# Kernel optimization log

Hardware: AMD Instinct MI355X
Metric: run time of the kernel (lower is better)

Reference implementation:

```python
import jax, jax.numpy as jnp
import numpy as np

T = 400      # timestamps (window length chosen == timestamps -> no padding branch)
D = 10000    # out_dimension (HDC hypervector dim)
TWO_PI = 2.0 * np.pi


def setup_inputs() -> dict:
    key = jax.random.key(0)
    ks = jax.random.split(key, 10)
    # monotonically increasing timestamps so jerk dt > 0
    t = jnp.cumsum(jax.random.uniform(ks[0], (T,), jnp.float32) + 0.5)
    xyz = jax.random.normal(ks[1], (T, 3), jnp.float32)
    inp = jnp.concatenate([t[:, None], xyz], axis=1)  # [T,4] = (t, x, y, z)
    W1 = jax.random.normal(ks[2], (D, T * 3), jnp.float32)
    b1 = jax.random.uniform(ks[3], (D,), jnp.float32, 0.0, TWO_PI)
    W2 = jax.random.normal(ks[4], (D, T * 3), jnp.float32)
    b2 = jax.random.uniform(ks[5], (D,), jnp.float32, 0.0, TWO_PI)
    W3 = jax.random.normal(ks[6], (D, T * 2), jnp.float32)
    b3 = jax.random.uniform(ks[7], (D,), jnp.float32, 0.0, TWO_PI)
    W4 = jax.random.normal(ks[8], (D, 3), jnp.float32)
    b4 = jax.random.uniform(ks[9], (D,), jnp.float32, 0.0, TWO_PI)
    return {"input": inp, "W1": W1, "b1": b1, "W2": W2, "b2": b2,
            "W3": W3, "b3": b3, "W4": W4, "b4": b4}


def _hypertangent(x, W, b):
    # HyperTangent random-feature embedding: tanh(W @ x + b)
    return jnp.tanh(W @ x + b)


def reference(input, W1, b1, W2, b2, W3, b3, W4, b4):
    t = input[:, 0] - input[0, 0]           # zero-base the time column
    xyz = input[:, 1:]                      # [T,3]
    sq = xyz * xyz
    mags = jnp.sqrt(jnp.sum(sq, axis=1))    # [T]
    energy = jnp.sum(sq, axis=0) / xyz.shape[0]  # [3]
    # vectorized jerk: (x_{i+1}-x_i)/(t_{i+1}-t_i), with a leading zeros row
    dt = (t[1:] - t[:-1])[:, None]          # [T-1,1]
    jerks = jnp.concatenate(
        [jnp.zeros((1, 3), input.dtype), (xyz[1:] - xyz[:-1]) / dt], axis=0)  # [T,3]
    jerk_mags = jnp.sqrt(jnp.sum(jerks * jerks, axis=1))  # [T]
    # window == timestamps -> no padding path
    features1 = jnp.concatenate([xyz[:, 0], xyz[:, 1], xyz[:, 2]])      # [3T]
    features2 = jnp.concatenate([jerks[:, 0], jerks[:, 1], jerks[:, 2]])  # [3T]
    features3 = jnp.concatenate([mags, jerk_mags])                       # [2T]
    hv1 = _hypertangent(features1, W1, b1)
    hv2 = _hypertangent(features2, W2, b2)
    hv3 = _hypertangent(features3, W3, b3)
    hv4 = _hypertangent(energy, W4, b4)
    return jnp.tanh(hv1 * hv4 + hv2 + hv3)  # [D]
```

## Files before the change

### kernel.cpp

```cpp
#include <hip/hip_runtime.h>
#include <hip/hip_bf16.h>
#include <math.h>

#define T_PTS 400
#define D_OUT 10000
#define L12   1200
#define L3    800
#define FEAT_TOTAL (L12 + L12 + L3 + 3)

__global__ __launch_bounds__(512)
void hdc_features_kernel(const float* __restrict__ in, float* __restrict__ feat) {
    __shared__ float red[3][8];
    const int tid = threadIdx.x;
    float ex = 0.f, ey = 0.f, ez = 0.f;

    if (tid < T_PTS) {
        const float4 cur = reinterpret_cast<const float4*>(in)[tid];
        const float x = cur.y, y = cur.z, z = cur.w;
        feat[tid]        = x;
        feat[400 + tid]  = y;
        feat[800 + tid]  = z;
        feat[2400 + tid] = sqrtf(x * x + y * y + z * z);
        ex = x * x; ey = y * y; ez = z * z;

        float jx = 0.f, jy = 0.f, jz = 0.f;
        if (tid > 0) {
            const float4 prev = reinterpret_cast<const float4*>(in)[tid - 1];
            const float dt = cur.x - prev.x;
            const float inv = 1.0f / dt;
            jx = (x - prev.y) * inv;
            jy = (y - prev.z) * inv;
            jz = (z - prev.w) * inv;
        }
        feat[1200 + tid] = jx;
        feat[1600 + tid] = jy;
        feat[2000 + tid] = jz;
        feat[2800 + tid] = sqrtf(jx * jx + jy * jy + jz * jz);
    }

    #pragma unroll
    for (int off = 32; off; off >>= 1) {
        ex += __shfl_down(ex, off, 64);
        ey += __shfl_down(ey, off, 64);
        ez += __shfl_down(ez, off, 64);
    }
    const int wave = tid >> 6, lane = tid & 63;
    if (lane == 0) { red[0][wave] = ex; red[1][wave] = ey; red[2][wave] = ez; }
    __syncthreads();
    if (tid == 0) {
        float sx = 0.f, sy = 0.f, sz = 0.f;
        #pragma unroll
        for (int w = 0; w < 8; ++w) { sx += red[0][w]; sy += red[1][w]; sz += red[2][w]; }
        const float invT = 1.0f / (float)T_PTS;
        feat[3200] = sx * invT;
        feat[3201] = sy * invT;
        feat[3202] = sz * invT;
    }
}

__global__ __launch_bounds__(256)
void hdc_gemv_kernel(const float* __restrict__ W1, const float* __restrict__ b1,
                     const float* __restrict__ W2, const float* __restrict__ b2,
                     const float* __restrict__ W3, const float* __restrict__ b3,
                     const float* __restrict__ W4, const float* __restrict__ b4,
                     const float* __restrict__ feat, float* __restrict__ out) {
    __shared__ float f[FEAT_TOTAL];
    const int tid = threadIdx.x;
    for (int k = tid; k < FEAT_TOTAL; k += 256) f[k] = feat[k];
    __syncthreads();

    const float e0 = f[3200], e1 = f[3201], e2 = f[3202];
    const int wave = tid >> 6, lane = tid & 63;
    const int d0 = blockIdx.x * 8 + wave * 2;
    const int d1 = d0 + 1;

    const float* __restrict__ f1 = f;
    const float* __restrict__ f2 = f + 1200;
    const float* __restrict__ f3 = f + 2400;

    const float* __restrict__ w1a = W1 + (size_t)d0 * L12;
    const float* __restrict__ w1b = W1 + (size_t)d1 * L12;
    const float* __restrict__ w2a = W2 + (size_t)d0 * L12;
    const float* __restrict__ w2b = W2 + (size_t)d1 * L12;
    const float* __restrict__ w3a = W3 + (size_t)d0 * L3;
    const float* __restrict__ w3b = W3 + (size_t)d1 * L3;

    float a1a = 0.f, a1b = 0.f, a2a = 0.f, a2b = 0.f, a3a = 0.f, a3b = 0.f;

    for (int k = lane * 4; k < L3; k += 256) {
        const float s1x = f1[k], s1y = f1[k + 1], s1z = f1[k + 2], s1w = f1[k + 3];
        const float s2x = f2[k], s2y = f2[k + 1], s2z = f2[k + 2], s2w = f2[k + 3];
        const float s3x = f3[k], s3y = f3[k + 1], s3z = f3[k + 2], s3w = f3[k + 3];
        const float4 va = *reinterpret_cast<const float4*>(w1a + k);
        const float4 vb = *reinterpret_cast<const float4*>(w1b + k);
        const float4 vc = *reinterpret_cast<const float4*>(w2a + k);
        const float4 vd = *reinterpret_cast<const float4*>(w2b + k);
        const float4 ve = *reinterpret_cast<const float4*>(w3a + k);
        const float4 vf = *reinterpret_cast<const float4*>(w3b + k);
        a1a += va.x * s1x + va.y * s1y + va.z * s1z + va.w * s1w;
        a1b += vb.x * s1x + vb.y * s1y + vb.z * s1z + vb.w * s1w;
        a2a += vc.x * s2x + vc.y * s2y + vc.z * s2z + vc.w * s2w;
        a2b += vd.x * s2x + vd.y * s2y + vd.z * s2z + vd.w * s2w;
        a3a += ve.x * s3x + ve.y * s3y + ve.z * s3z + ve.w * s3w;
        a3b += vf.x * s3x + vf.y * s3y + vf.z * s3z + vf.w * s3w;
    }
    for (int k = L3 + lane * 4; k < L12; k += 256) {
        const float s1x = f1[k], s1y = f1[k + 1], s1z = f1[k + 2], s1w = f1[k + 3];
        const float s2x = f2[k], s2y = f2[k + 1], s2z = f2[k + 2], s2w = f2[k + 3];
        const float4 va = *reinterpret_cast<const float4*>(w1a + k);
        const float4 vb = *reinterpret_cast<const float4*>(w1b + k);
        const float4 vc = *reinterpret_cast<const float4*>(w2a + k);
        const float4 vd = *reinterpret_cast<const float4*>(w2b + k);
        a1a += va.x * s1x + va.y * s1y + va.z * s1z + va.w * s1w;
        a1b += vb.x * s1x + vb.y * s1y + vb.z * s1z + vb.w * s1w;
        a2a += vc.x * s2x + vc.y * s2y + vc.z * s2z + vc.w * s2w;
        a2b += vd.x * s2x + vd.y * s2y + vd.z * s2z + vd.w * s2w;
    }

    #pragma unroll
    for (int off = 32; off; off >>= 1) {
        a1a += __shfl_down(a1a, off, 64);
        a1b += __shfl_down(a1b, off, 64);
        a2a += __shfl_down(a2a, off, 64);
        a2b += __shfl_down(a2b, off, 64);
        a3a += __shfl_down(a3a, off, 64);
        a3b += __shfl_down(a3b, off, 64);
    }

    if (lane == 0) {
        const float hv1a = tanhf(a1a + b1[d0]);
        const float hv2a = tanhf(a2a + b2[d0]);
        const float hv3a = tanhf(a3a + b3[d0]);
        const float hv4a = tanhf(W4[(size_t)d0 * 3 + 0] * e0 +
                                 W4[(size_t)d0 * 3 + 1] * e1 +
                                 W4[(size_t)d0 * 3 + 2] * e2 + b4[d0]);
        out[d0] = tanhf(hv1a * hv4a + hv2a + hv3a);

        const float hv1b = tanhf(a1b + b1[d1]);
        const float hv2b = tanhf(a2b + b2[d1]);
        const float hv3b = tanhf(a3b + b3[d1]);
        const float hv4b = tanhf(W4[(size_t)d1 * 3 + 0] * e0 +
                                 W4[(size_t)d1 * 3 + 1] * e1 +
                                 W4[(size_t)d1 * 3 + 2] * e2 + b4[d1]);
        out[d1] = tanhf(hv1b * hv4b + hv2b + hv3b);
    }
}

extern "C" void kernel_launch(void* const* d_in, const int* in_sizes, int n_in,
                              void* d_out, int out_size, void* d_ws, size_t ws_size,
                              hipStream_t stream) {
    const float* input = (const float*)d_in[0];
    const float* W1 = (const float*)d_in[1];
    const float* b1 = (const float*)d_in[2];
    const float* W2 = (const float*)d_in[3];
    const float* b2 = (const float*)d_in[4];
    const float* W3 = (const float*)d_in[5];
    const float* b3 = (const float*)d_in[6];
    const float* W4 = (const float*)d_in[7];
    const float* b4 = (const float*)d_in[8];
    float* out = (float*)d_out;
    float* feat = (float*)d_ws;

    hdc_features_kernel<<<1, 512, 0, stream>>>(input, feat);
    hdc_gemv_kernel<<<D_OUT / 8, 256, 0, stream>>>(W1, b1, W2, b2, W3, b3,
                                                   W4, b4, feat, out);
}
```

Before: 167.2 us.

## Issue all weight loads upfront into registers and pad shared features for float4 reads

The GEMV kernel now issues every row's float4 weight loads into register arrays before any arithmetic, putting all loads for a lane in flight at once instead of a loop-carried load/compute sequence. The shared feature vectors are copied into zero-padded, aligned segments so they can be read as float4 with no bounds checks. Launch bounds are raised to request four blocks per CU. The cost is much higher register pressure, which could cause spills or lower occupancy.

```diff
diff --git a/kernel.cpp b/kernel.cpp
--- a/kernel.cpp
+++ b/kernel.cpp
@@ -7,6 +7,12 @@
 #define L12   1200
 #define L3    800
 #define FEAT_TOTAL (L12 + L12 + L3 + 3)
+
+#define F1_OFF 0
+#define F2_OFF 1280
+#define F3_OFF 2560
+#define E_OFF  3584
+#define FS_TOTAL 3587
 
 __global__ __launch_bounds__(512)
 void hdc_features_kernel(const float* __restrict__ in, float* __restrict__ feat) {
@@ -58,25 +64,28 @@
     }
 }
 
-__global__ __launch_bounds__(256)
+__global__ __launch_bounds__(256, 4)
 void hdc_gemv_kernel(const float* __restrict__ W1, const float* __restrict__ b1,
                      const float* __restrict__ W2, const float* __restrict__ b2,
                      const float* __restrict__ W3, const float* __restrict__ b3,
                      const float* __restrict__ W4, const float* __restrict__ b4,
                      const float* __restrict__ feat, float* __restrict__ out) {
-    __shared__ float f[FEAT_TOTAL];
+    __shared__ float fs[FS_TOTAL];
     const int tid = threadIdx.x;
-    for (int k = tid; k < FEAT_TOTAL; k += 256) f[k] = feat[k];
+
+    for (int k = tid; k < 1280; k += 256) {
+        fs[F1_OFF + k] = (k < L12) ? feat[k] : 0.f;
+        fs[F2_OFF + k] = (k < L12) ? feat[L12 + k] : 0.f;
+    }
+    for (int k = tid; k < 1024; k += 256)
+        fs[F3_OFF + k] = (k < L3) ? feat[2400 + k] : 0.f;
+    if (tid < 3) fs[E_OFF + tid] = feat[3200 + tid];
     __syncthreads();
 
-    const float e0 = f[3200], e1 = f[3201], e2 = f[3202];
     const int wave = tid >> 6, lane = tid & 63;
     const int d0 = blockIdx.x * 8 + wave * 2;
     const int d1 = d0 + 1;
-
-    const float* __restrict__ f1 = f;
-    const float* __restrict__ f2 = f + 1200;
-    const float* __restrict__ f3 = f + 2400;
+    const int k0 = lane * 4;
 
     const float* __restrict__ w1a = W1 + (size_t)d0 * L12;
     const float* __restrict__ w1b = W1 + (size_t)d1 * L12;
@@ -85,36 +94,55 @@
     const float* __restrict__ w3a = W3 + (size_t)d0 * L3;
     const float* __restrict__ w3b = W3 + (size_t)d1 * L3;
 
+    const bool v12 = (lane < 44);
+    const bool v3  = (lane < 8);
+    const float4 z4 = make_float4(0.f, 0.f, 0.f, 0.f);
+
+    float4 r1a[5], r1b[5], r2a[5], r2b[5], r3a[4], r3b[4];
+    #pragma unroll
+    for (int i = 0; i < 4; ++i) {
+        const int k = k0 + 256 * i;
+        r1a[i] = *reinterpret_cast<const float4*>(w1a + k);
+        r1b[i] = *reinterpret_cast<const float4*>(w1b + k);
+        r2a[i] = *reinterpret_cast<const float4*>(w2a + k);
+        r2b[i] = *reinterpret_cast<const float4*>(w2b + k);
+    }
+    {
+        const int k = k0 + 1024;
+        r1a[4] = v12 ? *reinterpret_cast<const float4*>(w1a + k) : z4;
+        r1b[4] = v12 ? *reinterpret_cast<const float4*>(w1b + k) : z4;
+        r2a[4] = v12 ? *reinterpret_cast<const float4*>(w2a + k) : z4;
+        r2b[4] = v12 ? *reinterpret_cast<const float4*>(w2b + k) : z4;
+    }
+    #pragma unroll
+    for (int i = 0; i < 3; ++i) {
+        const int k = k0 + 256 * i;
+        r3a[i] = *reinterpret_cast<const float4*>(w3a + k);
+        r3b[i] = *reinterpret_cast<const float4*>(w3b + k);
+    }
+    {
+        const int k = k0 + 768;
+        r3a[3] = v3 ? *reinterpret_cast<const float4*>(w3a + k) : z4;
+        r3b[3] = v3 ? *reinterpret_cast<const float4*>(w3b + k) : z4;
+    }
+
     float a1a = 0.f, a1b = 0.f, a2a = 0.f, a2b = 0.f, a3a = 0.f, a3b = 0.f;
-
-    for (int k = lane * 4; k < L3; k += 256) {
-        const float s1x = f1[k], s1y = f1[k + 1], s1z = f1[k + 2], s1w = f1[k + 3];
-        const float s2x = f2[k], s2y = f2[k + 1], s2z = f2[k + 2], s2w = f2[k + 3];
-        const float s3x = f3[k], s3y = f3[k + 1], s3z = f3[k + 2], s3w = f3[k + 3];
-        const float4 va = *reinterpret_cast<const float4*>(w1a + k);
-        const float4 vb = *reinterpret_cast<const float4*>(w1b + k);
-        const float4 vc = *reinterpret_cast<const float4*>(w2a + k);
-        const float4 vd = *reinterpret_cast<const float4*>(w2b + k);
-        const float4 ve = *reinterpret_cast<const float4*>(w3a + k);
-        const float4 vf = *reinterpret_cast<const float4*>(w3b + k);
-        a1a += va.x * s1x + va.y * s1y + va.z * s1z + va.w * s1w;
-        a1b += vb.x * s1x + vb.y * s1y + vb.z * s1z + vb.w * s1w;
-        a2a += vc.x * s2x + vc.y * s2y + vc.z * s2z + vc.w * s2w;
-        a2b += vd.x * s2x + vd.y * s2y + vd.z * s2z + vd.w * s2w;
-        a3a += ve.x * s3x + ve.y * s3y + ve.z * s3z + ve.w * s3w;
-        a3b += vf.x * s3x + vf.y * s3y + vf.z * s3z + vf.w * s3w;
+    #pragma unroll
+    for (int i = 0; i < 5; ++i) {
+        const int k = k0 + 256 * i;
+        const float4 s1 = *reinterpret_cast<const float4*>(&fs[F1_OFF + k]);
+        const float4 s2 = *reinterpret_cast<const float4*>(&fs[F2_OFF + k]);
+        a1a += r1a[i].x * s1.x + r1a[i].y * s1.y + r1a[i].z * s1.z + r1a[i].w * s1.w;
+        a1b += r1b[i].x * s1.x + r1b[i].y * s1.y + r1b[i].z * s1.z + r1b[i].w * s1.w;
+        a2a += r2a[i].x * s2.x + r2a[i].y * s2.y + r2a[i].z * s2.z + r2a[i].w * s2.w;
+        a2b += r2b[i].x * s2.x + r2b[i].y * s2.y + r2b[i].z * s2.z + r2b[i].w * s2.w;
     }
-    for (int k = L3 + lane * 4; k < L12; k += 256) {
-        const float s1x = f1[k], s1y = f1[k + 1], s1z = f1[k + 2], s1w = f1[k + 3];
-        const float s2x = f2[k], s2y = f2[k + 1], s2z = f2[k + 2], s2w = f2[k + 3];
-        const float4 va = *reinterpret_cast<const float4*>(w1a + k);
-        const float4 vb = *reinterpret_cast<const float4*>(w1b + k);
-        const float4 vc = *reinterpret_cast<const float4*>(w2a + k);
-        const float4 vd = *reinterpret_cast<const float4*>(w2b + k);
-        a1a += va.x * s1x + va.y * s1y + va.z * s1z + va.w * s1w;
-        a1b += vb.x * s1x + vb.y * s1y + vb.z * s1z + vb.w * s1w;
-        a2a += vc.x * s2x + vc.y * s2y + vc.z * s2z + vc.w * s2w;
-        a2b += vd.x * s2x + vd.y * s2y + vd.z * s2z + vd.w * s2w;
+    #pragma unroll
+    for (int i = 0; i < 4; ++i) {
+        const int k = k0 + 256 * i;
+        const float4 s3 = *reinterpret_cast<const float4*>(&fs[F3_OFF + k]);
+        a3a += r3a[i].x * s3.x + r3a[i].y * s3.y + r3a[i].z * s3.z + r3a[i].w * s3.w;
+        a3b += r3b[i].x * s3.x + r3b[i].y * s3.y + r3b[i].z * s3.z + r3b[i].w * s3.w;
     }
 
     #pragma unroll
@@ -128,6 +156,7 @@
     }
 
     if (lane == 0) {
+        const float e0 = fs[E_OFF], e1 = fs[E_OFF + 1], e2 = fs[E_OFF + 2];
         const float hv1a = tanhf(a1a + b1[d0]);
         const float hv2a = tanhf(a2a + b2[d0]);
         const float hv3a = tanhf(a3a + b3[d0]);
```

After: 174.8 us. 1.05x slower.

## Issue all weight loads up front as one concatenated row per wave

Applied to the files above, without the earlier changes.

Each wave now handles a single output row and treats W1, W2 and W3 for that row as one 3200-element virtual row. All twelve float4 weight loads plus a float2 tail are issued before the shared-memory feature copy and barrier, so the global reads overlap the feature staging. Bias and W4 loads are also hoisted ahead of the reduction. This raises memory-level parallelism per thread and doubles the grid size, at the cost of more registers per thread and some per-segment select logic.

```diff
diff --git a/kernel.cpp b/kernel.cpp
--- a/kernel.cpp
+++ b/kernel.cpp
@@ -6,7 +6,8 @@
 #define D_OUT 10000
 #define L12   1200
 #define L3    800
-#define FEAT_TOTAL (L12 + L12 + L3 + 3)
+#define ROW   3200
+#define FEAT_TOTAL (ROW + 3)
 
 __global__ __launch_bounds__(512)
 void hdc_features_kernel(const float* __restrict__ in, float* __restrict__ feat) {
@@ -64,85 +65,77 @@
                      const float* __restrict__ W3, const float* __restrict__ b3,
                      const float* __restrict__ W4, const float* __restrict__ b4,
                      const float* __restrict__ feat, float* __restrict__ out) {
-    __shared__ float f[FEAT_TOTAL];
+    __shared__ __align__(16) float g[FEAT_TOTAL];
     const int tid = threadIdx.x;
-    for (int k = tid; k < FEAT_TOTAL; k += 256) f[k] = feat[k];
+    const int wave = tid >> 6, lane = tid & 63;
+    const int d = blockIdx.x * 4 + wave;
+    const int c0 = lane * 4;
+
+    const float* __restrict__ w1 = W1 + (size_t)d * L12;
+    const float* __restrict__ w2 = W2 + (size_t)d * L12;
+    const float* __restrict__ w3 = W3 + (size_t)d * L3;
+
+    float4 r[12];
+    #pragma unroll
+    for (int i = 0; i < 12; ++i) {
+        const int k = 256 * i + c0;
+        const float* p;
+        if (i < 4)       p = w1 + k;
+        else if (i == 4) p = (k < L12) ? (w1 + k) : (w2 + (k - L12));
+        else if (i < 9)  p = w2 + (k - L12);
+        else if (i == 9) p = (k < 2400) ? (w2 + (k - L12)) : (w3 + (k - 2400));
+        else             p = w3 + (k - 2400);
+        r[i] = *reinterpret_cast<const float4*>(p);
+    }
+    const float2 rt = *reinterpret_cast<const float2*>(w3 + (3072 - 2400) + 2 * lane);
+
+    {
+        float4* g4 = reinterpret_cast<float4*>(g);
+        const float4* feat4 = reinterpret_cast<const float4*>(feat);
+        for (int i = tid; i < ROW / 4; i += 256) g4[i] = feat4[i];
+        if (tid == 0) { g[3200] = feat[3200]; g[3201] = feat[3201]; g[3202] = feat[3202]; }
+    }
     __syncthreads();
 
-    const float e0 = f[3200], e1 = f[3201], e2 = f[3202];
-    const int wave = tid >> 6, lane = tid & 63;
-    const int d0 = blockIdx.x * 8 + wave * 2;
-    const int d1 = d0 + 1;
+    float acc1 = 0.f, acc2 = 0.f, acc3 = 0.f;
+    #pragma unroll
+    for (int i = 0; i < 12; ++i) {
+        const int k = 256 * i + c0;
+        const float4 s = *reinterpret_cast<const float4*>(&g[k]);
+        const float t = r[i].x * s.x + r[i].y * s.y + r[i].z * s.z + r[i].w * s.w;
+        if (i < 4)       acc1 += t;
+        else if (i == 4) { acc1 += (k < L12) ? t : 0.f; acc2 += (k < L12) ? 0.f : t; }
+        else if (i < 9)  acc2 += t;
+        else if (i == 9) { acc2 += (k < 2400) ? t : 0.f; acc3 += (k < 2400) ? 0.f : t; }
+        else             acc3 += t;
+    }
+    {
+        const int k = 3072 + 2 * lane;
+        acc3 += rt.x * g[k] + rt.y * g[k + 1];
+    }
 
-    const float* __restrict__ f1 = f;
-    const float* __restrict__ f2 = f + 1200;
-    const float* __restrict__ f3 = f + 2400;
-
-    const float* __restrict__ w1a = W1 + (size_t)d0 * L12;
-    const float* __restrict__ w1b = W1 + (size_t)d1 * L12;
-    const float* __restrict__ w2a = W2 + (size_t)d0 * L12;
-    const float* __restrict__ w2b = W2 + (size_t)d1 * L12;
-    const float* __restrict__ w3a = W3 + (size_t)d0 * L3;
-    const float* __restrict__ w3b = W3 + (size_t)d1 * L3;
-
-    float a1a = 0.f, a1b = 0.f, a2a = 0.f, a2b = 0.f, a3a = 0.f, a3b = 0.f;
-
-    for (int k = lane * 4; k < L3; k += 256) {
-        const float s1x = f1[k], s1y = f1[k + 1], s1z = f1[k + 2], s1w = f1[k + 3];
-        const float s2x = f2[k], s2y = f2[k + 1], s2z = f2[k + 2], s2w = f2[k + 3];
-        const float s3x = f3[k], s3y = f3[k + 1], s3z = f3[k + 2], s3w = f3[k + 3];
-        const float4 va = *reinterpret_cast<const float4*>(w1a + k);
-        const float4 vb = *reinterpret_cast<const float4*>(w1b + k);
-        const float4 vc = *reinterpret_cast<const float4*>(w2a + k);
-        const float4 vd = *reinterpret_cast<const float4*>(w2b + k);
-        const float4 ve = *reinterpret_cast<const float4*>(w3a + k);
-        const float4 vf = *reinterpret_cast<const float4*>(w3b + k);
-        a1a += va.x * s1x + va.y * s1y + va.z * s1z + va.w * s1w;
-        a1b += vb.x * s1x + vb.y * s1y + vb.z * s1z + vb.w * s1w;
-        a2a += vc.x * s2x + vc.y * s2y + vc.z * s2z + vc.w * s2w;
-        a2b += vd.x * s2x + vd.y * s2y + vd.z * s2z + vd.w * s2w;
-        a3a += ve.x * s3x + ve.y * s3y + ve.z * s3z + ve.w * s3w;
-        a3b += vf.x * s3x + vf.y * s3y + vf.z * s3z + vf.w * s3w;
-    }
-    for (int k = L3 + lane * 4; k < L12; k += 256) {
-        const float s1x = f1[k], s1y = f1[k + 1], s1z = f1[k + 2], s1w = f1[k + 3];
-        const float s2x = f2[k], s2y = f2[k + 1], s2z = f2[k + 2], s2w = f2[k + 3];
-        const float4 va = *reinterpret_cast<const float4*>(w1a + k);
-        const float4 vb = *reinterpret_cast<const float4*>(w1b + k);
-        const float4 vc = *reinterpret_cast<const float4*>(w2a + k);
-        const float4 vd = *reinterpret_cast<const float4*>(w2b + k);
-        a1a += va.x * s1x + va.y * s1y + va.z * s1z + va.w * s1w;
-        a1b += vb.x * s1x + vb.y * s1y + vb.z * s1z + vb.w * s1w;
-        a2a += vc.x * s2x + vc.y * s2y + vc.z * s2z + vc.w * s2w;
-        a2b += vd.x * s2x + vd.y * s2y + vd.z * s2z + vd.w * s2w;
+    float bb1 = 0.f, bb2 = 0.f, bb3 = 0.f, bb4 = 0.f, w40 = 0.f, w41 = 0.f, w42 = 0.f;
+    if (lane == 0) {
+        bb1 = b1[d]; bb2 = b2[d]; bb3 = b3[d]; bb4 = b4[d];
+        w40 = W4[(size_t)d * 3 + 0];
+        w41 = W4[(size_t)d * 3 + 1];
+        w42 = W4[(size_t)d * 3 + 2];
     }
 
     #pragma unroll
     for (int off = 32; off; off >>= 1) {
-        a1a += __shfl_down(a1a, off, 64);
-        a1b += __shfl_down(a1b, off, 64);
-        a2a += __shfl_down(a2a, off, 64);
-        a2b += __shfl_down(a2b, off, 64);
-        a3a += __shfl_down(a3a, off, 64);
-        a3b += __shfl_down(a3b, off, 64);
+        acc1 += __shfl_down(acc1, off, 64);
+        acc2 += __shfl_down(acc2, off, 64);
+        acc3 += __shfl_down(acc3, off, 64);
     }
 
     if (lane == 0) {
-        const float hv1a = tanhf(a1a + b1[d0]);
-        const float hv2a = tanhf(a2a + b2[d0]);
-        const float hv3a = tanhf(a3a + b3[d0]);
-        const float hv4a = tanhf(W4[(size_t)d0 * 3 + 0] * e0 +
-                                 W4[(size_t)d0 * 3 + 1] * e1 +
-                                 W4[(size_t)d0 * 3 + 2] * e2 + b4[d0]);
-        out[d0] = tanhf(hv1a * hv4a + hv2a + hv3a);
-
-        const float hv1b = tanhf(a1b + b1[d1]);
-        const float hv2b = tanhf(a2b + b2[d1]);
-        const float hv3b = tanhf(a3b + b3[d1]);
-        const float hv4b = tanhf(W4[(size_t)d1 * 3 + 0] * e0 +
-                                 W4[(size_t)d1 * 3 + 1] * e1 +
-                                 W4[(size_t)d1 * 3 + 2] * e2 + b4[d1]);
-        out[d1] = tanhf(hv1b * hv4b + hv2b + hv3b);
+        const float e0 = g[3200], e1 = g[3201], e2 = g[3202];
+        const float hv1 = tanhf(acc1 + bb1);
+        const float hv2 = tanhf(acc2 + bb2);
+        const float hv3 = tanhf(acc3 + bb3);
+        const float hv4 = tanhf(w40 * e0 + w41 * e1 + w42 * e2 + bb4);
+        out[d] = tanhf(hv1 * hv4 + hv2 + hv3);
     }
 }
 
@@ -162,6 +155,6 @@
     float* feat = (float*)d_ws;
 
     hdc_features_kernel<<<1, 512, 0, stream>>>(input, feat);
-    hdc_gemv_kernel<<<D_OUT / 8, 256, 0, stream>>>(W1, b1, W2, b2, W3, b3,
+    hdc_gemv_kernel<<<D_OUT / 4, 256, 0, stream>>>(W1, b1, W2, b2, W3, b3,
                                                    W4, b4, feat, out);
 }
```

Measured after the change: 163.8 us. -2.1%, faster.
